# Optimization experiments

Hardware: AMD Instinct MI355X
Metric: run time of the kernel (lower is better)

The kernel has to match this reference:

```python
import jax, jax.numpy as jnp
import numpy as np

B, N, T, D = 16, 30, 50, 4
K, H, M, NH = 4, 128, 128, 128
E = N * (N - 1)  # 870


def setup_inputs() -> dict:
    key = jax.random.key(0)
    ks = jax.random.split(key, 12)
    # one-hot receiver / sender matrices for fully connected graph (no self loops)
    pairs = np.array([(i, j) for i in range(N) for j in range(N) if i != j])
    eye = np.eye(N, dtype=np.float32)
    rel_rec = jnp.asarray(eye[pairs[:, 0]])   # [E, N]
    rel_send = jnp.asarray(eye[pairs[:, 1]])  # [E, N]
    s = 0.1
    return {
        "inputs": jax.random.normal(ks[0], (B, N, T, D), jnp.float32),
        "rel_type": jax.random.uniform(ks[1], (B, E, K), jnp.float32),
        "rel_rec": rel_rec,
        "rel_send": rel_send,
        "W1": jax.random.normal(ks[2], (K, 2 * D, H), jnp.float32) * s,
        "b1": jax.random.normal(ks[3], (K, H), jnp.float32) * s,
        "W2": jax.random.normal(ks[4], (K, H, M), jnp.float32) * s,
        "b2": jax.random.normal(ks[5], (K, M), jnp.float32) * s,
        "oW1": jax.random.normal(ks[6], (D + M, NH), jnp.float32) * s,
        "ob1": jax.random.normal(ks[7], (NH,), jnp.float32) * s,
        "oW2": jax.random.normal(ks[8], (NH, NH), jnp.float32) * s,
        "ob2": jax.random.normal(ks[9], (NH,), jnp.float32) * s,
        "oW3": jax.random.normal(ks[10], (NH, D), jnp.float32) * s,
        "ob3": jax.random.normal(ks[11], (D,), jnp.float32) * s,
        "pred_steps": 1,
    }


def _single_step(x, rt, rel_rec, rel_send, W1, b1, W2, b2, oW1, ob1, oW2, ob2, oW3, ob3):
    # x: [B, Ts, N, D], rt: [B, Ts, E, K]
    recv = jnp.einsum('en,btnd->bted', rel_rec, x)
    send = jnp.einsum('en,btnd->bted', rel_send, x)
    pre_msg = jnp.concatenate([recv, send], axis=-1)           # [B,Ts,E,2D]
    all_msgs = jnp.zeros(pre_msg.shape[:-1] + (M,), x.dtype)
    for k in range(K):  # small fixed set of structurally distinct MLPs
        msg = jax.nn.relu(pre_msg @ W1[k] + b1[k])
        msg = jax.nn.relu(msg @ W2[k] + b2[k])
        all_msgs = all_msgs + msg * rt[..., k:k + 1]
    agg = jnp.einsum('btef,en->btnf', all_msgs, rel_rec)       # scatter-sum to receivers
    aug = jnp.concatenate([x, agg], axis=-1)                    # [B,Ts,N,D+M]
    h = jax.nn.relu(aug @ oW1 + ob1)
    h = jax.nn.relu(h @ oW2 + ob2)
    return x + (h @ oW3 + ob3)


def reference(inputs, rel_type, rel_rec, rel_send, W1, b1, W2, b2,
              oW1, ob1, oW2, ob2, oW3, ob3, pred_steps):
    x = jnp.transpose(inputs, (0, 2, 1, 3))                    # [B,T,N,D]
    Tt = x.shape[1]
    rt = jnp.broadcast_to(rel_type[:, None], (rel_type.shape[0], Tt) + rel_type.shape[1:])
    last_pred = x[:, 0::pred_steps]
    curr_rt = rt[:, 0::pred_steps]
    preds = []
    for _ in range(pred_steps):
        last_pred = _single_step(last_pred, curr_rt, rel_rec, rel_send,
                                 W1, b1, W2, b2, oW1, ob1, oW2, ob2, oW3, ob3)
        preds.append(last_pred)
    Ts = preds[0].shape[1]
    out = jnp.stack(preds, axis=2).reshape(x.shape[0], Ts * pred_steps, x.shape[2], x.shape[3])
    pred_all = out[:, :Tt - 1]
    return jnp.transpose(pred_all, (0, 2, 1, 3))               # [B,N,T-1,D]
```

## Files before the change

### kernel.cpp

```cpp
#include <hip/hip_runtime.h>

typedef __bf16 bf16_t;
typedef __bf16 bf16x8 __attribute__((ext_vector_type(8)));
typedef __bf16 bf16x4 __attribute__((ext_vector_type(4)));
typedef float  f32x4  __attribute__((ext_vector_type(4)));

#define NB 16
#define NN 30
#define NT 50
#define ND 4
#define NK 4
#define NE 870

#define C_INPUTS   0
#define C_RELTYPE  96000
#define C_B2       152192
#define C_OB1      152704
#define C_OB2      152832
#define C_OW3      152960
#define C_OB3      153472
#define C_W1F      153480
#define C_W2F      169864
#define C_OW1F     235400
#define C_OW2F     255880
#define AGG_BYTE_OFF (1u << 20)

__device__ __forceinline__ bf16x8 bzero8() {
  bf16x8 z;
#pragma unroll
  for (int j = 0; j < 8; ++j) z[j] = (bf16_t)0.0f;
  return z;
}

__device__ __forceinline__ f32x4 make4(float a, float b, float c, float d) {
  f32x4 v; v[0] = a; v[1] = b; v[2] = c; v[3] = d; return v;
}

__device__ __forceinline__ void pack_store4(bf16_t* dst, f32x4 a) {
  bf16x4 v;
  v[0] = (bf16_t)fmaxf(a[0], 0.0f);
  v[1] = (bf16_t)fmaxf(a[1], 0.0f);
  v[2] = (bf16_t)fmaxf(a[2], 0.0f);
  v[3] = (bf16_t)fmaxf(a[3], 0.0f);
  *(bf16x4*)dst = v;
}

__device__ __forceinline__ int detect_isbf16(const void* p) {
  const unsigned short* w = (const unsigned short*)p;
  int c = 0;
#pragma unroll 4
  for (int i = 0; i < 256; i += 2) {
    const int e = (w[i] >> 7) & 0xFF;
    if (e >= 100 && e <= 150) ++c;
  }
  return c >= 96;
}

__device__ __forceinline__ float ldf(const void* src, int idx, int isbf) {
  return isbf ? (float)((const bf16_t*)src)[idx] : ((const float*)src)[idx];
}

__device__ __forceinline__ void conv_arr(const void* src, bf16_t* dst, int n,
                                         int isbf, int gtid, int gsz) {
  if (isbf) {
    const unsigned short* s = (const unsigned short*)src;
    unsigned short* d = (unsigned short*)dst;
    for (int i = gtid; i < n; i += gsz) d[i] = s[i];
  } else {
    const float* s = (const float*)src;
    for (int i = gtid; i < n; i += gsz) dst[i] = (bf16_t)s[i];
  }
}

__global__ void convert_kernel(const void* inputs, const void* rel_type,
                               const void* W1, const void* b1,
                               const void* W2, const void* b2,
                               const void* oW1, const void* ob1,
                               const void* oW2, const void* ob2,
                               const void* oW3, const void* ob3,
                               void* ws)
{
  __shared__ int sflag;
  if (threadIdx.x == 0) sflag = detect_isbf16(inputs);
  __syncthreads();
  const int isbf = sflag;
  if (blockIdx.x == 0 && threadIdx.x == 0) *(int*)ws = isbf;
  bf16_t* cb = (bf16_t*)((char*)ws + 16);
  const int gtid = blockIdx.x * blockDim.x + threadIdx.x;
  const int gsz  = gridDim.x * blockDim.x;

  conv_arr(inputs,   cb + C_INPUTS,  96000, isbf, gtid, gsz);
  conv_arr(rel_type, cb + C_RELTYPE, 55680, isbf, gtid, gsz);
  conv_arr(b2,  cb + C_B2,  512, isbf, gtid, gsz);
  conv_arr(ob1, cb + C_OB1, 128, isbf, gtid, gsz);
  conv_arr(ob2, cb + C_OB2, 128, isbf, gtid, gsz);
  conv_arr(oW3, cb + C_OW3, 512, isbf, gtid, gsz);
  conv_arr(ob3, cb + C_OB3, 4,   isbf, gtid, gsz);

  for (int i = gtid; i < 16384; i += gsz) {
    const int j = i & 7, lm = (i >> 3) & 15, quad = (i >> 7) & 3;
    const int ct = (i >> 9) & 7, k = (i >> 12) & 3;
    float v = 0.0f;
    if (quad == 0)                 v = ldf(W1, k * 1024 + j * 128 + ct * 16 + lm, isbf);
    else if (quad == 1 && j == 0)  v = ldf(b1, k * 128 + ct * 16 + lm, isbf);
    cb[C_W1F + i] = (bf16_t)v;
  }
  for (int i = gtid; i < 65536; i += gsz) {
    const int j = i & 7;
    const int l64 = (i >> 3) & 63;
    const int ct = (i >> 9) & 7, kc = (i >> 12) & 3, k = (i >> 14) & 3;
    const int quad = l64 >> 4, lm = l64 & 15;
    const int kk = kc * 32 + quad * 8 + j;
    cb[C_W2F + i] = (bf16_t)ldf(W2, k * 16384 + kk * 128 + ct * 16 + lm, isbf);
  }
  for (int i = gtid; i < 20480; i += gsz) {
    const int j = i & 7, lm = (i >> 3) & 15, quad = (i >> 7) & 3;
    const int rem = i >> 9;
    const int kc = rem % 5, ct = rem / 5;
    const int kk = kc * 32 + quad * 8 + j;
    float v = 0.0f;
    if (kk < 132) v = ldf(oW1, kk * 128 + ct * 16 + lm, isbf);
    cb[C_OW1F + i] = (bf16_t)v;
  }
  for (int i = gtid; i < 16384; i += gsz) {
    const int j = i & 7, lm = (i >> 3) & 15, quad = (i >> 7) & 3;
    const int kc = (i >> 9) & 3, ct = (i >> 11) & 7;
    const int kk = kc * 32 + quad * 8 + j;
    cb[C_OW2F + i] = (bf16_t)ldf(oW2, kk * 128 + ct * 16 + lm, isbf);
  }
}

struct EdgeSmem {
  bf16_t h[8192];
  union { bf16_t m[128 * 68]; float aggf[2048]; } mb;
  bf16_t sfrag[7168];
  bf16_t xl[128];
};

__device__ __forceinline__ void agg_step(const EdgeSmem& s, int chunkid, int ctbase,
                                         int quad, int lm, int lane, int mychunk,
                                         f32x4* aggacc) {
  const bf16x8 sa = *(const bf16x8*)&s.sfrag[(chunkid * 64 + lane) * 8];
#pragma unroll
  for (int c = 0; c < 4; ++c) {
    const bf16x8 mbf = *(const bf16x8*)&s.mb.m[((ctbase + c) * 16 + lm) * 68 + mychunk * 32 + quad * 8];
    aggacc[c] = __builtin_amdgcn_mfma_f32_16x16x32_bf16(sa, mbf, aggacc[c], 0, 0, 0);
  }
}

__global__ __launch_bounds__(256)
void edge_kernel(const bf16_t* __restrict__ inputs,
                 const bf16_t* __restrict__ rel_type,
                 const bf16_t* __restrict__ w1f_g,
                 const bf16_t* __restrict__ w2f_g,
                 const bf16_t* __restrict__ b2c,
                 float* __restrict__ aggbuf)
{
  __shared__ EdgeSmem s;
  const int tid  = threadIdx.x;
  const int bid  = blockIdx.x;
  const int nhalf = bid & 1;
  const int bt   = bid >> 1;
  const int b    = bt / NT;
  const int t    = bt - b * NT;
  const int wave = tid >> 6;
  const int lane = tid & 63;
  const int quad = lane >> 4;
  const int lm   = lane & 15;
  const int ctbase  = (wave & 1) * 4;
  const int spair   = (wave >> 1) * 2;
  const int mychunk = wave >> 1;

  if (tid < 30) {
    *(uint2*)&s.xl[tid * 4] = *(const uint2*)&inputs[((b * NN + tid) * NT + t) * ND];
  }
  for (int i = tid; i < 896; i += 256) *(bf16x8*)&s.sfrag[i * 8] = bzero8();
  __syncthreads();

  const int e0g = b * NE + nhalf * 435;
  f32x4 aggacc[4];
#pragma unroll
  for (int c = 0; c < 4; ++c) aggacc[c] = make4(0.f, 0.f, 0.f, 0.f);

#pragma unroll 1
  for (int k = 0; k < NK; ++k) {
    bf16x8 w1r[4];
    bf16x8 w2r[4][4];
    float  b2s[4];
#pragma unroll
    for (int c = 0; c < 4; ++c) {
      const int ct = ctbase + c;
      w1r[c] = *(const bf16x8*)&w1f_g[(((k * 8 + ct) * 4 + quad) * 16 + lm) * 8];
#pragma unroll
      for (int kc = 0; kc < 4; ++kc)
        w2r[c][kc] = *(const bf16x8*)&w2f_g[((((k * 4 + kc) * 8) + ct) * 64 + quad * 16 + lm) * 8];
      b2s[c] = (float)b2c[k * 128 + ct * 16 + lm];
    }
    for (int i = tid; i < 435; i += 256) {
      const int n = i / 29;
      const int slot = (((i >> 5) * 4 + ((i >> 3) & 3)) * 16 + n) * 8 + (i & 7);
      s.sfrag[slot] = rel_type[(e0g + i) * 4 + k];
    }

#pragma unroll 1
    for (int tt = 0; tt < 7; ++tt) {
      if (tt > 0) agg_step(s, (tt - 1) * 2 + mychunk, ctbase, quad, lm, lane, mychunk, aggacc);

#pragma unroll
      for (int si = 0; si < 2; ++si) {
        const int strip = spair + si;
        const int rr = strip * 16 + lm;
        const int e  = tt * 64 + rr;
        bf16x8 pm = bzero8();
        if (quad == 0) {
          if (e < 435) {
            const int recv = nhalf * 15 + e / 29;
            const int j29  = e % 29;
            const int send = j29 + (j29 >= recv);
            union { uint2 u2[2]; bf16x8 v; } c;
            c.u2[0] = *(const uint2*)&s.xl[recv * 4];
            c.u2[1] = *(const uint2*)&s.xl[send * 4];
            pm = c.v;
          }
        } else if (quad == 1) {
          pm[0] = (bf16_t)1.0f;
        }
        const f32x4 z4 = make4(0.0f, 0.0f, 0.0f, 0.0f);
#pragma unroll
        for (int c = 0; c < 4; ++c) {
          const int ct = ctbase + c;
          f32x4 a1 = __builtin_amdgcn_mfma_f32_16x16x32_bf16(w1r[c], pm, z4, 0, 0, 0);
          const int qr = 2 * (ct & 1) + (quad >> 1);
          pack_store4(&s.h[((strip * 4 + (ct >> 1)) * 64 + qr * 16 + lm) * 8 + 4 * (quad & 1)], a1);
        }
      }
      __syncthreads();

#pragma unroll
      for (int si = 0; si < 2; ++si) {
        const int strip = spair + si;
        bf16x8 af[4];
#pragma unroll
        for (int kc = 0; kc < 4; ++kc)
          af[kc] = *(const bf16x8*)&s.h[((strip * 4 + kc) * 64 + quad * 16 + lm) * 8];
#pragma unroll
        for (int c = 0; c < 4; ++c) {
          f32x4 acc = make4(b2s[c], b2s[c], b2s[c], b2s[c]);
#pragma unroll
          for (int kc = 0; kc < 4; ++kc)
            acc = __builtin_amdgcn_mfma_f32_16x16x32_bf16(af[kc], w2r[c][kc], acc, 0, 0, 0);
          pack_store4(&s.mb.m[((ctbase + c) * 16 + lm) * 68 + strip * 16 + quad * 4], acc);
        }
      }
      __syncthreads();
    }
    agg_step(s, 12 + mychunk, ctbase, quad, lm, lane, mychunk, aggacc);
    __syncthreads();
  }

  for (int i = tid; i < 2048; i += 256) s.mb.aggf[i] = 0.0f;
  __syncthreads();
#pragma unroll
  for (int c = 0; c < 4; ++c)
#pragma unroll
    for (int r = 0; r < 4; ++r)
      atomicAdd(&s.mb.aggf[(quad * 4 + r) * 128 + (ctbase + c) * 16 + lm], aggacc[c][r]);
  __syncthreads();
  for (int i = tid; i < 15 * 128; i += 256) {
    const int r = i >> 7, col = i & 127;
    aggbuf[(size_t)(bt * NN + nhalf * 15 + r) * 128 + col] = s.mb.aggf[r * 128 + col];
  }
}

struct NodeSmem {
  bf16_t h1[64 * 136];
  bf16_t h2[64 * 136];
  bf16_t xres[64 * 4];
  float  b1f[128];
  float  b2f[128];
  float  w3f[128 * 4];
  float  b3f[4];
};

__global__ __launch_bounds__(256)
void node_kernel(const bf16_t* __restrict__ inputs,
                 const bf16_t* __restrict__ ow1f_g, const bf16_t* __restrict__ ob1,
                 const bf16_t* __restrict__ ow2f_g, const bf16_t* __restrict__ ob2,
                 const bf16_t* __restrict__ oW3, const bf16_t* __restrict__ ob3,
                 const int* __restrict__ flagptr,
                 const float* __restrict__ aggbuf,
                 void* __restrict__ outp)
{
  __shared__ NodeSmem s;
  const int tid  = threadIdx.x;
  const int wave = tid >> 6;
  const int lane = tid & 63;
  const int quad = lane >> 4;
  const int lm   = lane & 15;
  const int row  = wave * 16 + lm;
  const int r0   = blockIdx.x * 64;
  const int isbf = *flagptr;

  if (tid < 64) {
    const int r  = r0 + tid;
    const int n  = r % NN;
    const int bt = r / NN;
    const int t  = bt % NT;
    const int b  = bt / NT;
    *(uint2*)&s.xres[tid * 4] = *(const uint2*)&inputs[((b * NN + n) * NT + t) * ND];
  }
  if (tid < 128) s.b1f[tid] = (float)ob1[tid];
  else           s.b2f[tid - 128] = (float)ob2[tid - 128];
  if (tid < 4) s.b3f[tid] = (float)ob3[tid];
  for (int i = tid; i < 512; i += 256) s.w3f[i] = (float)oW3[i];
  __syncthreads();

  bf16x8 bfa[5];
  {
    const float* aggrow = aggbuf + (size_t)(r0 + row) * 128;
    float tmp[8];
    if (quad == 0) {
#pragma unroll
      for (int j = 0; j < 4; ++j) tmp[j] = (float)s.xres[row * 4 + j];
      const float4 a = *(const float4*)(aggrow);
      tmp[4] = a.x; tmp[5] = a.y; tmp[6] = a.z; tmp[7] = a.w;
    } else {
      const int c0 = quad * 8 - 4;
      const float4 a = *(const float4*)(aggrow + c0);
      const float4 d = *(const float4*)(aggrow + c0 + 4);
      tmp[0] = a.x; tmp[1] = a.y; tmp[2] = a.z; tmp[3] = a.w;
      tmp[4] = d.x; tmp[5] = d.y; tmp[6] = d.z; tmp[7] = d.w;
    }
#pragma unroll
    for (int j = 0; j < 8; ++j) bfa[0][j] = (bf16_t)tmp[j];
#pragma unroll
    for (int kc = 1; kc < 4; ++kc) {
      const int c0 = kc * 32 + quad * 8 - 4;
      const float4 a = *(const float4*)(aggrow + c0);
      const float4 d = *(const float4*)(aggrow + c0 + 4);
      tmp[0] = a.x; tmp[1] = a.y; tmp[2] = a.z; tmp[3] = a.w;
      tmp[4] = d.x; tmp[5] = d.y; tmp[6] = d.z; tmp[7] = d.w;
#pragma unroll
      for (int j = 0; j < 8; ++j) bfa[kc][j] = (bf16_t)tmp[j];
    }
    if (quad == 0) {
      const float4 a = *(const float4*)(aggrow + 124);
      tmp[0] = a.x; tmp[1] = a.y; tmp[2] = a.z; tmp[3] = a.w;
      tmp[4] = 0.f; tmp[5] = 0.f; tmp[6] = 0.f; tmp[7] = 0.f;
#pragma unroll
      for (int j = 0; j < 8; ++j) bfa[4][j] = (bf16_t)tmp[j];
    } else bfa[4] = bzero8();
  }

#pragma unroll
  for (int ct = 0; ct < 8; ++ct) {
    const int nb = ct * 16 + quad * 4;
    f32x4 acc = make4(s.b1f[nb], s.b1f[nb + 1], s.b1f[nb + 2], s.b1f[nb + 3]);
#pragma unroll
    for (int kc = 0; kc < 5; ++kc) {
      const bf16x8 w = *(const bf16x8*)&ow1f_g[(((ct * 5 + kc) * 4 + quad) * 16 + lm) * 8];
      acc = __builtin_amdgcn_mfma_f32_16x16x32_bf16(w, bfa[kc], acc, 0, 0, 0);
    }
    pack_store4(&s.h1[row * 136 + ct * 16 + quad * 4], acc);
  }

  bf16x8 af[4];
#pragma unroll
  for (int kc = 0; kc < 4; ++kc)
    af[kc] = *(const bf16x8*)&s.h1[row * 136 + kc * 32 + quad * 8];

#pragma unroll
  for (int ct = 0; ct < 8; ++ct) {
    const int mb = ct * 16 + quad * 4;
    f32x4 acc = make4(s.b2f[mb], s.b2f[mb + 1], s.b2f[mb + 2], s.b2f[mb + 3]);
#pragma unroll
    for (int kc = 0; kc < 4; ++kc) {
      const bf16x8 w = *(const bf16x8*)&ow2f_g[(((ct * 4 + kc) * 4 + quad) * 16 + lm) * 8];
      acc = __builtin_amdgcn_mfma_f32_16x16x32_bf16(w, af[kc], acc, 0, 0, 0);
    }
    pack_store4(&s.h2[row * 136 + ct * 16 + quad * 4], acc);
  }

  {
    const int rloc = tid >> 2;
    const int d    = tid & 3;
    float a3 = s.b3f[d];
#pragma unroll
    for (int g = 0; g < 16; ++g) {
      const bf16x8 hv = *(const bf16x8*)&s.h2[rloc * 136 + g * 8];
#pragma unroll
      for (int j = 0; j < 8; ++j)
        a3 += (float)hv[j] * s.w3f[(g * 8 + j) * 4 + d];
    }
    a3 += (float)s.xres[rloc * 4 + d];
    const int r  = r0 + rloc;
    const int n  = r % NN;
    const int bt = r / NN;
    const int t  = bt % NT;
    const int b  = bt / NT;
    if (t < NT - 1) {
      const int oidx = ((b * NN + n) * (NT - 1) + t) * ND + d;
      if (isbf) ((bf16_t*)outp)[oidx] = (bf16_t)a3;
      else      ((float*)outp)[oidx]  = a3;
    }
  }
}

extern "C" void kernel_launch(void* const* d_in, const int* in_sizes, int n_in,
                              void* d_out, int out_size, void* d_ws, size_t ws_size,
                              hipStream_t stream) {
  char* ws = (char*)d_ws;
  bf16_t* cb = (bf16_t*)(ws + 16);
  float* aggbuf = (float*)(ws + AGG_BYTE_OFF);

  convert_kernel<<<dim3(256), dim3(256), 0, stream>>>(
      d_in[0], d_in[1], d_in[4], d_in[5], d_in[6], d_in[7],
      d_in[8], d_in[9], d_in[10], d_in[11], d_in[12], d_in[13], d_ws);

  edge_kernel<<<dim3(NB * NT * 2), dim3(256), 0, stream>>>(
      cb + C_INPUTS, cb + C_RELTYPE, cb + C_W1F, cb + C_W2F,
      cb + C_B2, aggbuf);

  node_kernel<<<dim3((NB * NT * NN) / 64), dim3(256), 0, stream>>>(
      cb + C_INPUTS, cb + C_OW1F, cb + C_OB1, cb + C_OW2F, cb + C_OB2,
      cb + C_OW3, cb + C_OB3, (const int*)d_ws, aggbuf, d_out);
}
```

Measured before the change: 384.9 us.

## Feed second-layer MFMA output directly into aggregation MFMA in registers

The edge kernel no longer writes the layer-2 message tile to shared memory to reduce it later with a separate aggregation step. Each wave now applies ReLU to its MFMA accumulator, packs it as a bf16 operand and immediately runs the aggregation MFMA against a relaid-out rel_type fragment. This drops the message staging buffer, its LDS traffic and the extra agg_step calls and barriers per relation type, shrinking shared memory. In exchange the aggregation MFMA uses only 4 of its 8 K slots, so half of each instruction multiplies zeros.

```diff
diff --git a/kernel.cpp b/kernel.cpp
--- a/kernel.cpp
+++ b/kernel.cpp
@@ -131,22 +131,10 @@
 }
 
 struct EdgeSmem {
-  bf16_t h[8192];
-  union { bf16_t m[128 * 68]; float aggf[2048]; } mb;
+  union { bf16_t h[8192]; float aggf[2048]; } u;
   bf16_t sfrag[7168];
   bf16_t xl[128];
 };
-
-__device__ __forceinline__ void agg_step(const EdgeSmem& s, int chunkid, int ctbase,
-                                         int quad, int lm, int lane, int mychunk,
-                                         f32x4* aggacc) {
-  const bf16x8 sa = *(const bf16x8*)&s.sfrag[(chunkid * 64 + lane) * 8];
-#pragma unroll
-  for (int c = 0; c < 4; ++c) {
-    const bf16x8 mbf = *(const bf16x8*)&s.mb.m[((ctbase + c) * 16 + lm) * 68 + mychunk * 32 + quad * 8];
-    aggacc[c] = __builtin_amdgcn_mfma_f32_16x16x32_bf16(sa, mbf, aggacc[c], 0, 0, 0);
-  }
-}
 
 __global__ __launch_bounds__(256)
 void edge_kernel(const bf16_t* __restrict__ inputs,
@@ -167,9 +155,8 @@
   const int lane = tid & 63;
   const int quad = lane >> 4;
   const int lm   = lane & 15;
-  const int ctbase  = (wave & 1) * 4;
-  const int spair   = (wave >> 1) * 2;
-  const int mychunk = wave >> 1;
+  const int ctbase = (wave & 1) * 4;
+  const int spair  = (wave >> 1) * 2;
 
   if (tid < 30) {
     *(uint2*)&s.xl[tid * 4] = *(const uint2*)&inputs[((b * NN + tid) * NT + t) * ND];
@@ -197,15 +184,12 @@
       b2s[c] = (float)b2c[k * 128 + ct * 16 + lm];
     }
     for (int i = tid; i < 435; i += 256) {
-      const int n = i / 29;
-      const int slot = (((i >> 5) * 4 + ((i >> 3) & 3)) * 16 + n) * 8 + (i & 7);
+      const int slot = ((i >> 4) * 64 + ((i >> 2) & 3) * 16 + i / 29) * 4 + (i & 3);
       s.sfrag[slot] = rel_type[(e0g + i) * 4 + k];
     }
 
 #pragma unroll 1
     for (int tt = 0; tt < 7; ++tt) {
-      if (tt > 0) agg_step(s, (tt - 1) * 2 + mychunk, ctbase, quad, lm, lane, mychunk, aggacc);
-
 #pragma unroll
       for (int si = 0; si < 2; ++si) {
         const int strip = spair + si;
@@ -231,7 +215,7 @@
           const int ct = ctbase + c;
           f32x4 a1 = __builtin_amdgcn_mfma_f32_16x16x32_bf16(w1r[c], pm, z4, 0, 0, 0);
           const int qr = 2 * (ct & 1) + (quad >> 1);
-          pack_store4(&s.h[((strip * 4 + (ct >> 1)) * 64 + qr * 16 + lm) * 8 + 4 * (quad & 1)], a1);
+          pack_store4(&s.u.h[((strip * 4 + (ct >> 1)) * 64 + qr * 16 + lm) * 8 + 4 * (quad & 1)], a1);
         }
       }
       __syncthreads();
@@ -242,33 +226,41 @@
         bf16x8 af[4];
 #pragma unroll
         for (int kc = 0; kc < 4; ++kc)
-          af[kc] = *(const bf16x8*)&s.h[((strip * 4 + kc) * 64 + quad * 16 + lm) * 8];
+          af[kc] = *(const bf16x8*)&s.u.h[((strip * 4 + kc) * 64 + quad * 16 + lm) * 8];
+        bf16x8 sa = bzero8();
+        {
+          const bf16x4 s4 = *(const bf16x4*)&s.sfrag[((tt * 4 + strip) * 64 + lane) * 4];
+          sa[0] = s4[0]; sa[1] = s4[1]; sa[2] = s4[2]; sa[3] = s4[3];
+        }
 #pragma unroll
         for (int c = 0; c < 4; ++c) {
           f32x4 acc = make4(b2s[c], b2s[c], b2s[c], b2s[c]);
 #pragma unroll
           for (int kc = 0; kc < 4; ++kc)
             acc = __builtin_amdgcn_mfma_f32_16x16x32_bf16(af[kc], w2r[c][kc], acc, 0, 0, 0);
-          pack_store4(&s.mb.m[((ctbase + c) * 16 + lm) * 68 + strip * 16 + quad * 4], acc);
+          bf16x8 mb = bzero8();
+          mb[0] = (bf16_t)fmaxf(acc[0], 0.0f);
+          mb[1] = (bf16_t)fmaxf(acc[1], 0.0f);
+          mb[2] = (bf16_t)fmaxf(acc[2], 0.0f);
+          mb[3] = (bf16_t)fmaxf(acc[3], 0.0f);
+          aggacc[c] = __builtin_amdgcn_mfma_f32_16x16x32_bf16(sa, mb, aggacc[c], 0, 0, 0);
         }
       }
       __syncthreads();
     }
-    agg_step(s, 12 + mychunk, ctbase, quad, lm, lane, mychunk, aggacc);
-    __syncthreads();
-  }
-
-  for (int i = tid; i < 2048; i += 256) s.mb.aggf[i] = 0.0f;
+  }
+
+  for (int i = tid; i < 2048; i += 256) s.u.aggf[i] = 0.0f;
   __syncthreads();
 #pragma unroll
   for (int c = 0; c < 4; ++c)
 #pragma unroll
     for (int r = 0; r < 4; ++r)
-      atomicAdd(&s.mb.aggf[(quad * 4 + r) * 128 + (ctbase + c) * 16 + lm], aggacc[c][r]);
+      atomicAdd(&s.u.aggf[(quad * 4 + r) * 128 + (ctbase + c) * 16 + lm], aggacc[c][r]);
   __syncthreads();
   for (int i = tid; i < 15 * 128; i += 256) {
     const int r = i >> 7, col = i & 127;
-    aggbuf[(size_t)(bt * NN + nhalf * 15 + r) * 128 + col] = s.mb.aggf[r * 128 + col];
+    aggbuf[(size_t)(bt * NN + nhalf * 15 + r) * 128 + col] = s.u.aggf[r * 128 + col];
   }
 }
 
```

After: 345.5 us. 10.2% less time.
